# Performance work log

Measured on AMD Instinct MI355X. Metric: run time of the kernel, lower is better.

## Reference

```python
import jax, jax.numpy as jnp
import numpy as np

K_WEIGHT = 1.7  # K passed in original forward: w(t, H, 1.7)
B_EXP = 2.5     # default exponent b in w()


def setup_inputs() -> dict:
    key = jax.random.key(0)
    k1, k2 = jax.random.split(key)
    B, H, D = 512, 2048, 64
    pred = jax.random.normal(k1, (B, H, D), dtype=jnp.float32)
    targ = jax.random.normal(k2, (B, H, D), dtype=jnp.float32)
    return {"pred": pred, "targ": targ}


def reference(pred, targ):
    # pred, targ: [B, H, D]
    B, H, D = pred.shape
    # t_i = number of nonzero entries of targ[i, :, 1] along horizon
    t = jnp.sum((targ[:, :, 1] != 0).astype(pred.dtype), axis=1)  # [B]
    # w(t, T=H, K=1.7, b=2.5) = 1 + (K-1) * (t/(H-1))**b
    weight = 1.0 + (K_WEIGHT - 1.0) * (t / (H - 1)) ** B_EXP      # [B]
    idx = t.astype(jnp.int32) - 1                                  # [B], scatter row per sample
    # Only channel 0 of the squared error is ever used (loss[:, :, :1]);
    # the [B,H,1]*[B,H,D] broadcast + sum over D is equivalent to *D.
    loss0 = (pred[:, :, 0] - targ[:, :, 0]) ** 2                   # [B, H]
    gathered = jnp.take_along_axis(loss0, idx[:, None], axis=1)[:, 0]  # [B]
    weighted_loss = jnp.mean(gathered * weight * D)
    return weighted_loss
```

## Files before the change

### kernel.cpp

```cpp
#include <hip/hip_runtime.h>


#define BB 512
#define HH 2048
#define DD 64
#define CHUNKS 4
#define HPC (HH / CHUNKS)

__global__ __launch_bounds__(256) void wsl4_count(
    const float* __restrict__ targ, int* __restrict__ partial)
{
    const int c   = blockIdx.x;
    const int i   = blockIdx.y;
    const int tid = threadIdx.x;

    const float* p = targ + (size_t)i * HH * DD + (size_t)c * HPC * DD + 1;

    const float a = p[(size_t)tid * DD];
    const float b = p[((size_t)tid + 256) * DD];
    int cnt = (a != 0.0f ? 1 : 0) + (b != 0.0f ? 1 : 0);

#pragma unroll
    for (int off = 32; off > 0; off >>= 1)
        cnt += __shfl_down(cnt, off, 64);

    __shared__ int s[4];
    if ((tid & 63) == 0) s[tid >> 6] = cnt;
    __syncthreads();

    if (tid == 0) partial[i * CHUNKS + c] = s[0] + s[1] + s[2] + s[3];
}

__global__ __launch_bounds__(512) void wsl4_final(
    const float* __restrict__ pred, const float* __restrict__ targ,
    const int* __restrict__ partial, float* __restrict__ out)
{
    const int i = threadIdx.x;

    const int4 t4 = *(const int4*)(partial + i * CHUNKS);
    const int t = t4.x + t4.y + t4.z + t4.w;

    const float ratio = (float)t / (float)(HH - 1);
    const float w = 1.0f + 0.7f * powf(ratio, 2.5f);

    int idx = t - 1;
    idx = idx < 0 ? 0 : (idx > HH - 1 ? HH - 1 : idx);

    const size_t base = ((size_t)i * HH + (size_t)idx) * DD;
    const float d = pred[base] - targ[base];
    float val = d * d * w * ((float)DD / (float)BB);

#pragma unroll
    for (int off = 32; off > 0; off >>= 1)
        val += __shfl_down(val, off, 64);

    __shared__ float sf[8];
    if ((i & 63) == 0) sf[i >> 6] = val;
    __syncthreads();

    if (i == 0) {
        float tot = 0.0f;
#pragma unroll
        for (int k = 0; k < 8; ++k) tot += sf[k];
        out[0] = tot;
    }
}

extern "C" void kernel_launch(void* const* d_in, const int* in_sizes, int n_in,
                              void* d_out, int out_size, void* d_ws, size_t ws_size,
                              hipStream_t stream)
{
    const float* pred = (const float*)d_in[0];
    const float* targ = (const float*)d_in[1];
    float* out = (float*)d_out;
    int* partial = (int*)d_ws;

    dim3 grid(CHUNKS, BB);
    wsl4_count<<<grid, 256, 0, stream>>>(targ, partial);
    wsl4_final<<<1, 512, 0, stream>>>(pred, targ, partial, out);
}
```

Measured before the change: 29.66 us.

## Fuse count and final reduction into one kernel via last-block atomic ticket

Merges the two launches into one kernel. Each block publishes its partial count and bumps a global atomic ticket, and the block that arrives last performs the gather, weighting and final sum. This removes the second kernel launch and the gap between kernels. In exchange it adds atomic traffic and relies on a counter in the workspace that is never reset, handled by a modulo check, which assumes the counter starts at zero.

```diff
diff --git a/kernel.cpp b/kernel.cpp
--- a/kernel.cpp
+++ b/kernel.cpp
@@ -6,16 +6,19 @@
 #define DD 64
 #define CHUNKS 4
 #define HPC (HH / CHUNKS)
+#define NBLK (BB * CHUNKS)
 
-__global__ __launch_bounds__(256) void wsl4_count(
-    const float* __restrict__ targ, int* __restrict__ partial)
+__global__ __launch_bounds__(256) void wsl4_fused(
+    const float* __restrict__ pred,
+    const float* __restrict__ targ,
+    int* __restrict__ ws,
+    float* __restrict__ out)
 {
     const int c   = blockIdx.x;
     const int i   = blockIdx.y;
     const int tid = threadIdx.x;
 
     const float* p = targ + (size_t)i * HH * DD + (size_t)c * HPC * DD + 1;
-
     const float a = p[(size_t)tid * DD];
     const float b = p[((size_t)tid + 256) * DD];
     int cnt = (a != 0.0f ? 1 : 0) + (b != 0.0f ? 1 : 0);
@@ -25,45 +28,52 @@
         cnt += __shfl_down(cnt, off, 64);
 
     __shared__ int s[4];
+    __shared__ int flag;
+    if (tid == 0) flag = 0;
     if ((tid & 63) == 0) s[tid >> 6] = cnt;
     __syncthreads();
 
-    if (tid == 0) partial[i * CHUNKS + c] = s[0] + s[1] + s[2] + s[3];
-}
+    if (tid == 0) {
+        const int total = s[0] + s[1] + s[2] + s[3];
+        __hip_atomic_store(&ws[1 + i * CHUNKS + c], total,
+                           __ATOMIC_RELAXED, __HIP_MEMORY_SCOPE_AGENT);
+        const unsigned old = __hip_atomic_fetch_add(
+            (unsigned*)&ws[0], 1u, __ATOMIC_ACQ_REL, __HIP_MEMORY_SCOPE_AGENT);
+        if (((old + 1u) & (unsigned)(NBLK - 1)) == 0u) flag = 1;
+    }
+    __syncthreads();
+    if (flag == 0) return;
 
-__global__ __launch_bounds__(512) void wsl4_final(
-    const float* __restrict__ pred, const float* __restrict__ targ,
-    const int* __restrict__ partial, float* __restrict__ out)
-{
-    const int i = threadIdx.x;
+    float acc = 0.0f;
+#pragma unroll
+    for (int k = 0; k < 2; ++k) {
+        const int smp = tid + k * 256;
+        int t = 0;
+#pragma unroll
+        for (int q = 0; q < CHUNKS; ++q)
+            t += __hip_atomic_load(&ws[1 + smp * CHUNKS + q],
+                                   __ATOMIC_RELAXED, __HIP_MEMORY_SCOPE_AGENT);
 
-    const int4 t4 = *(const int4*)(partial + i * CHUNKS);
-    const int t = t4.x + t4.y + t4.z + t4.w;
+        const float ratio = (float)t * (1.0f / (float)(HH - 1));
+        const float w = 1.0f + 0.7f * powf(ratio, 2.5f);
 
-    const float ratio = (float)t / (float)(HH - 1);
-    const float w = 1.0f + 0.7f * powf(ratio, 2.5f);
+        int idx = t - 1;
+        idx = idx < 0 ? 0 : (idx > HH - 1 ? HH - 1 : idx);
 
-    int idx = t - 1;
-    idx = idx < 0 ? 0 : (idx > HH - 1 ? HH - 1 : idx);
-
-    const size_t base = ((size_t)i * HH + (size_t)idx) * DD;
-    const float d = pred[base] - targ[base];
-    float val = d * d * w * ((float)DD / (float)BB);
+        const size_t base = ((size_t)smp * HH + (size_t)idx) * DD;
+        const float d = pred[base] - targ[base];
+        acc += d * d * w;
+    }
+    acc *= (float)DD / (float)BB;
 
 #pragma unroll
     for (int off = 32; off > 0; off >>= 1)
-        val += __shfl_down(val, off, 64);
+        acc += __shfl_down(acc, off, 64);
 
-    __shared__ float sf[8];
-    if ((i & 63) == 0) sf[i >> 6] = val;
+    __shared__ float sf[4];
+    if ((tid & 63) == 0) sf[tid >> 6] = acc;
     __syncthreads();
-
-    if (i == 0) {
-        float tot = 0.0f;
-#pragma unroll
-        for (int k = 0; k < 8; ++k) tot += sf[k];
-        out[0] = tot;
-    }
+    if (tid == 0) out[0] = sf[0] + sf[1] + sf[2] + sf[3];
 }
 
 extern "C" void kernel_launch(void* const* d_in, const int* in_sizes, int n_in,
@@ -72,10 +82,7 @@
 {
     const float* pred = (const float*)d_in[0];
     const float* targ = (const float*)d_in[1];
-    float* out = (float*)d_out;
-    int* partial = (int*)d_ws;
 
     dim3 grid(CHUNKS, BB);
-    wsl4_count<<<grid, 256, 0, stream>>>(targ, partial);
-    wsl4_final<<<1, 512, 0, stream>>>(pred, targ, partial, out);
+    wsl4_fused<<<grid, 256, 0, stream>>>(pred, targ, (int*)d_ws, (float*)d_out);
 }
```

Result: slower. 82.25 us (+177.3%).
